# Kernel optimization log

Hardware: AMD Instinct MI355X
Metric: run time of the kernel (lower is better)

The kernel has to match this reference:

```python
import jax, jax.numpy as jnp
import numpy as np

B, L, D_MODEL, D_STATE, D_CONV, EXPAND = 2, 1024, 1024, 16, 4, 2
D_INNER = D_MODEL * EXPAND


def setup_inputs() -> dict:
    key = jax.random.key(0)
    ks = jax.random.split(key, 8)
    s = lambda fan: 1.0 / np.sqrt(fan)
    x = jax.random.normal(ks[0], (B, L, D_MODEL), jnp.float32)
    in_proj_w = jax.random.normal(ks[1], (D_MODEL, 2 * D_INNER), jnp.float32) * s(D_MODEL)
    conv_w = jax.random.normal(ks[2], (D_INNER, 1, D_CONV), jnp.float32) * s(D_CONV)
    conv_b = jax.random.normal(ks[3], (D_INNER,), jnp.float32) * 0.01
    x_proj_w = jax.random.normal(ks[4], (D_INNER, 2 * D_STATE + D_INNER), jnp.float32) * s(D_INNER)
    dt_proj_w = jax.random.normal(ks[5], (D_INNER, D_INNER), jnp.float32) * s(D_INNER)
    dt_proj_b = jax.random.normal(ks[6], (D_INNER,), jnp.float32) * 0.01
    A_log = jnp.log(jnp.tile(jnp.arange(1, D_STATE + 1, dtype=jnp.float32)[None, :], (D_INNER, 1)))
    D = jnp.ones((D_INNER,), jnp.float32)
    out_proj_w = jax.random.normal(ks[7], (D_INNER, D_MODEL), jnp.float32) * s(D_INNER)
    return {"x": x, "in_proj_w": in_proj_w, "conv_w": conv_w, "conv_b": conv_b,
            "x_proj_w": x_proj_w, "dt_proj_w": dt_proj_w, "dt_proj_b": dt_proj_b,
            "A_log": A_log, "D": D, "out_proj_w": out_proj_w}


def _mamba_forward(x, in_proj_w, conv_w, conv_b, x_proj_w, dt_proj_w, dt_proj_b, A_log, D, out_proj_w):
    Bb, Ll, _ = x.shape
    d_inner, _, d_conv = conv_w.shape
    d_state = A_log.shape[1]
    # input projection and gate split
    xz = x @ in_proj_w                       # [B, L, 2*Di]
    x_inner, z = jnp.split(xz, 2, axis=-1)   # each [B, L, Di]
    # causal depthwise conv (left pad k-1, truncate to L == torch pad+slice)
    xc = jnp.transpose(x_inner, (0, 2, 1))   # [B, Di, L]
    xc = jax.lax.conv_general_dilated(
        xc, conv_w, window_strides=(1,), padding=[(d_conv - 1, 0)],
        dimension_numbers=("NCH", "OIH", "NCH"), feature_group_count=d_inner)
    xc = xc + conv_b[None, :, None]
    u = jax.nn.silu(jnp.transpose(xc, (0, 2, 1)))  # [B, L, Di]
    # SSM parameter projections
    ssm = u @ x_proj_w                        # [B, L, 2N+Di]
    B_ssm = ssm[..., :d_state]                # [B, L, N]
    C_ssm = ssm[..., d_state:2 * d_state]     # [B, L, N]
    dt = jax.nn.softplus(ssm[..., 2 * d_state:] @ dt_proj_w + dt_proj_b)  # [B, L, Di]
    A_real = -jnp.exp(A_log)                  # [Di, N]
    # selective scan over sequence (recurrence via lax.scan)
    def step(h, inp):
        dt_t, B_t, u_t = inp                  # [B,Di], [B,N], [B,Di]
        dA = jnp.exp(dt_t[..., None] * A_real)            # [B, Di, N]
        dBu = dt_t[..., None] * B_t[:, None, :] * u_t[..., None]
        h = dA * h + dBu
        return h, h
    h0 = jnp.zeros((Bb, d_inner, d_state), x.dtype)
    xs = (jnp.swapaxes(dt, 0, 1), jnp.swapaxes(B_ssm, 0, 1), jnp.swapaxes(u, 0, 1))
    _, states = jax.lax.scan(step, h0, xs)    # [L, B, Di, N]
    y = jnp.einsum("lbdn,lbn->lbd", states, jnp.swapaxes(C_ssm, 0, 1))
    y = jnp.swapaxes(y, 0, 1) + D * u         # skip connection
    y = y * jax.nn.silu(z)                    # gating
    return y @ out_proj_w                     # [B, L, d_model]


def reference(x, in_proj_w, conv_w, conv_b, x_proj_w, dt_proj_w, dt_proj_b, A_log, D, out_proj_w):
    return _mamba_forward(x, in_proj_w, conv_w, conv_b, x_proj_w, dt_proj_w, dt_proj_b, A_log, D, out_proj_w)
```

## Files before the change

kernel.cpp:

```cpp
#include <hip/hip_runtime.h>
#include <hip/hip_bf16.h>

#define BB 2
#define LL 1024
#define DMODEL 1024
#define DINNER 2048
#define DSTATE 16
#define DCONV 4
#define MM (BB * LL)
#define N_XZ 4096
#define N_SSM 2080
#define N_SSM_PAD 2176
#define CCH 32
#define LCH 32

typedef __hip_bfloat16 bf16;
typedef short bf16x8 __attribute__((ext_vector_type(8)));
typedef float f32x4 __attribute__((ext_vector_type(4)));

__device__ __forceinline__ void load16_lds(const bf16* g, bf16* l) {
    __builtin_amdgcn_global_load_lds(
        (const __attribute__((address_space(1))) void*)g,
        (__attribute__((address_space(3))) void*)l,
        16, 0, 0);
}

__global__ void cvt_kernel(const float* __restrict__ in, bf16* __restrict__ out, int n) {
    int i = blockIdx.x * blockDim.x + threadIdx.x;
    if (i < n) out[i] = __float2bfloat16(in[i]);
}

__global__ void transpose_cvt_kernel(const float* __restrict__ in, bf16* __restrict__ out,
                                     int K, int N) {
    __shared__ float tile[32][33];
    const int nb = blockIdx.x * 32, kb = blockIdx.y * 32;
    const int tx = threadIdx.x & 31;
    const int ty = threadIdx.x >> 5;
    #pragma unroll
    for (int i = 0; i < 32; i += 8) {
        int k = kb + ty + i, n = nb + tx;
        tile[ty + i][tx] = (k < K && n < N) ? in[(size_t)k * N + n] : 0.f;
    }
    __syncthreads();
    #pragma unroll
    for (int i = 0; i < 32; i += 8) {
        int n = nb + ty + i, k = kb + tx;
        if (n < N && k < K) out[(size_t)n * K + k] = __float2bfloat16(tile[tx][ty + i]);
    }
}

#define TM 128
#define TN 64
#define TK 32
template<int EPI>
__global__ __launch_bounds__(256) void mfma_gemm(
    const bf16* __restrict__ A, int lda,
    const bf16* __restrict__ Wt, int ldw,
    float* __restrict__ Cf, bf16* __restrict__ Cb, int ldc,
    const float* __restrict__ bias,
    int N, int K)
{
    __shared__ __align__(16) bf16 As[TM * TK];
    __shared__ __align__(16) bf16 Bs[TN * TK];
    const int tid = threadIdx.x;
    const int wave = tid >> 6, lane = tid & 63;
    const int wm = (wave >> 1) * 64, wn = (wave & 1) * 32;
    const int m0 = blockIdx.y * TM, n0 = blockIdx.x * TN;
    const int lm = lane & 15;
    const int kq = lane >> 4;

    const int srow = lane >> 2;
    const int scol = (lane & 3) * 8;

    f32x4 acc[4][2] = {};

    const bf16* Aw0 = A + (size_t)(m0 + wave * 16 + srow) * lda + scol;
    const bf16* Aw1 = A + (size_t)(m0 + wave * 16 + 64 + srow) * lda + scol;
    const bf16* Bw  = Wt + (size_t)(n0 + wave * 16 + srow) * ldw + scol;
    bf16* As0 = &As[(wave * 16) * TK];
    bf16* As1 = &As[(wave * 16 + 64) * TK];
    bf16* Bs0 = &Bs[(wave * 16) * TK];

    for (int k0 = 0; k0 < K; k0 += TK) {
        load16_lds(Aw0 + k0, As0);
        load16_lds(Aw1 + k0, As1);
        load16_lds(Bw + k0, Bs0);
        __syncthreads();

        bf16x8 af[4], bfr[2];
        #pragma unroll
        for (int i = 0; i < 4; ++i)
            af[i] = *(const bf16x8*)(&As[(wm + i * 16 + lm) * TK + kq * 8]);
        #pragma unroll
        for (int j = 0; j < 2; ++j)
            bfr[j] = *(const bf16x8*)(&Bs[(wn + j * 16 + lm) * TK + kq * 8]);
        #pragma unroll
        for (int i = 0; i < 4; ++i)
            #pragma unroll
            for (int j = 0; j < 2; ++j)
                acc[i][j] = __builtin_amdgcn_mfma_f32_16x16x32_bf16(af[i], bfr[j], acc[i][j], 0, 0, 0);
        __syncthreads();
    }

    #pragma unroll
    for (int i = 0; i < 4; ++i) {
        #pragma unroll
        for (int j = 0; j < 2; ++j) {
            int gcol = n0 + wn + j * 16 + lm;
            if ((EPI == 0 || EPI == 3) && gcol >= N) continue;
            #pragma unroll
            for (int r = 0; r < 4; ++r) {
                int grow = m0 + wm + i * 16 + kq * 4 + r;
                float v = acc[i][j][r];
                if (EPI == 1) {
                    v += bias[gcol];
                    v = (v > 20.f) ? v : log1pf(__expf(v));
                    Cf[(size_t)grow * ldc + gcol] = v;
                } else if (EPI == 2) {
                    Cf[(size_t)grow * ldc + gcol] = v;
                } else if (EPI == 3) {
                    if (gcol < 32) Cf[(size_t)grow * 32 + gcol] = v;
                    else           Cb[(size_t)grow * ldc + gcol] = __float2bfloat16(v);
                } else {
                    Cb[(size_t)grow * ldc + gcol] = __float2bfloat16(v);
                }
            }
        }
    }
}

__global__ void conv_silu_kernel(const bf16* __restrict__ xz,
                                 const float* __restrict__ conv_w,
                                 const float* __restrict__ conv_b,
                                 bf16* __restrict__ u)
{
    int idx = blockIdx.x * blockDim.x + threadIdx.x;
    if (idx >= BB * LL * DINNER) return;
    int d = idx & (DINNER - 1);
    int l = (idx >> 11) & (LL - 1);
    int b = idx >> 21;
    float acc = conv_b[d];
    #pragma unroll
    for (int j = 0; j < DCONV; ++j) {
        int ll = l - (DCONV - 1) + j;
        if (ll >= 0) {
            float xv = (float)xz[((size_t)(b * LL + ll)) * N_XZ + d];
            acc = fmaf(conv_w[d * DCONV + j], xv, acc);
        }
    }
    u[idx] = __float2bfloat16(acc / (1.f + __expf(-acc)));
}

__global__ __launch_bounds__(256) void scan_phase_a(
    const float* __restrict__ dt, const bf16* __restrict__ u,
    const float* __restrict__ BC,
    const float* __restrict__ A_log,
    float* __restrict__ chunkP, float* __restrict__ chunkH)
{
    const int d = blockIdx.x * 256 + threadIdx.x;
    const int c = blockIdx.y, b = blockIdx.z;
    const int l0 = c * LCH;

    float A[DSTATE];
    {
        const f32x4* ap = (const f32x4*)(A_log + d * DSTATE);
        #pragma unroll
        for (int q = 0; q < 4; ++q) {
            f32x4 v = ap[q];
            #pragma unroll
            for (int r = 0; r < 4; ++r) A[q * 4 + r] = -__expf(v[r]);
        }
    }
    float h[DSTATE];
    #pragma unroll
    for (int n = 0; n < DSTATE; ++n) h[n] = 0.f;
    float sdt = 0.f;

    const float* dtp = dt + ((size_t)b * LL + l0) * DINNER + d;
    const bf16* up = u + ((size_t)b * LL + l0) * DINNER + d;
    const float* bcp = BC + ((size_t)b * LL + l0) * 32;

    #pragma unroll 2
    for (int i = 0; i < LCH; ++i) {
        float dtv = *dtp;
        float uv  = (float)*up;
        float du  = dtv * uv;
        f32x4 Bv[4];
        #pragma unroll
        for (int q = 0; q < 4; ++q) Bv[q] = *(const f32x4*)(bcp + q * 4);
        #pragma unroll
        for (int n = 0; n < DSTATE; ++n) {
            float a = __expf(dtv * A[n]);
            h[n] = fmaf(a, h[n], du * Bv[n >> 2][n & 3]);
        }
        sdt += dtv;
        dtp += DINNER; up += DINNER; bcp += 32;
    }

    size_t idx = (((size_t)b * CCH + c) * DINNER + d) * DSTATE;
    #pragma unroll
    for (int q = 0; q < 4; ++q) {
        f32x4 pv, hv;
        #pragma unroll
        for (int r = 0; r < 4; ++r) { pv[r] = __expf(A[q * 4 + r] * sdt); hv[r] = h[q * 4 + r]; }
        *(f32x4*)(chunkP + idx + q * 4) = pv;
        *(f32x4*)(chunkH + idx + q * 4) = hv;
    }
}

__global__ __launch_bounds__(256) void scan_phase_p(
    const float* __restrict__ chunkP, float* __restrict__ chunkH)
{
    int gid = blockIdx.x * 256 + threadIdx.x;
    int n = gid & 15;
    int d = (gid >> 4) & (DINNER - 1);
    int b = gid >> 15;
    const size_t stride = (size_t)DINNER * DSTATE;
    size_t idx = ((size_t)b * CCH * DINNER + d) * DSTATE + n;
    float H = 0.f;
    for (int c = 0; c < CCH; ++c) {
        float P  = chunkP[idx];
        float hl = chunkH[idx];
        chunkH[idx] = H;
        H = fmaf(P, H, hl);
        idx += stride;
    }
}

__global__ __launch_bounds__(256) void scan_phase_b(
    const float* __restrict__ dt, bf16* __restrict__ u,
    const float* __restrict__ BC, const bf16* __restrict__ xz,
    const float* __restrict__ A_log, const float* __restrict__ Dp,
    const float* __restrict__ chunkH)
{
    const int d = blockIdx.x * 256 + threadIdx.x;
    const int c = blockIdx.y, b = blockIdx.z;
    const int l0 = c * LCH;

    float A[DSTATE];
    {
        const f32x4* ap = (const f32x4*)(A_log + d * DSTATE);
        #pragma unroll
        for (int q = 0; q < 4; ++q) {
            f32x4 v = ap[q];
            #pragma unroll
            for (int r = 0; r < 4; ++r) A[q * 4 + r] = -__expf(v[r]);
        }
    }
    const float Dd = Dp[d];
    float h[DSTATE];
    {
        size_t idx = (((size_t)b * CCH + c) * DINNER + d) * DSTATE;
        #pragma unroll
        for (int q = 0; q < 4; ++q) {
            f32x4 v = *(const f32x4*)(chunkH + idx + q * 4);
            #pragma unroll
            for (int r = 0; r < 4; ++r) h[q * 4 + r] = v[r];
        }
    }

    const float* dtp = dt + ((size_t)b * LL + l0) * DINNER + d;
    bf16* up = u + ((size_t)b * LL + l0) * DINNER + d;
    const float* bcp = BC + ((size_t)b * LL + l0) * 32;
    const bf16* zp = xz + ((size_t)b * LL + l0) * N_XZ + DINNER + d;

    #pragma unroll 2
    for (int i = 0; i < LCH; ++i) {
        float dtv = *dtp;
        float uv  = (float)*up;
        float du  = dtv * uv;
        f32x4 Bv[4], Cv[4];
        #pragma unroll
        for (int q = 0; q < 4; ++q) {
            Bv[q] = *(const f32x4*)(bcp + q * 4);
            Cv[q] = *(const f32x4*)(bcp + 16 + q * 4);
        }
        float acc = 0.f;
        #pragma unroll
        for (int n = 0; n < DSTATE; ++n) {
            float a = __expf(dtv * A[n]);
            h[n] = fmaf(a, h[n], du * Bv[n >> 2][n & 3]);
            acc = fmaf(h[n], Cv[n >> 2][n & 3], acc);
        }
        float zv = (float)*zp;
        acc = fmaf(Dd, uv, acc);
        acc *= zv / (1.f + __expf(-zv));
        *up = __float2bfloat16(acc);
        dtp += DINNER; up += DINNER; bcp += 32; zp += N_XZ;
    }
}

extern "C" void kernel_launch(void* const* d_in, const int* in_sizes, int n_in,
                              void* d_out, int out_size, void* d_ws, size_t ws_size,
                              hipStream_t stream) {
    const float* x         = (const float*)d_in[0];
    const float* in_proj_w = (const float*)d_in[1];
    const float* conv_w    = (const float*)d_in[2];
    const float* conv_b    = (const float*)d_in[3];
    const float* x_proj_w  = (const float*)d_in[4];
    const float* dt_proj_w = (const float*)d_in[5];
    const float* dt_proj_b = (const float*)d_in[6];
    const float* A_log     = (const float*)d_in[7];
    const float* Dp        = (const float*)d_in[8];
    const float* out_proj_w= (const float*)d_in[9];
    float* out = (float*)d_out;

    char* p = (char*)d_ws;
    float* dt   = (float*)p;                          p += (size_t)MM * DINNER * 4;
    bf16*  xbf  = (bf16*)dt;
    bf16*  xz   = (bf16*)p;                           p += (size_t)MM * N_XZ * 2;
    bf16*  u    = (bf16*)p;                           p += (size_t)MM * DINNER * 2;
    bf16*  ssm  = (bf16*)p;                           p += (size_t)MM * N_SSM * 2;
    bf16*  Wt1  = (bf16*)p;                           p += (size_t)N_XZ * DMODEL * 2;
    bf16*  Wt2  = (bf16*)p;                           p += (size_t)N_SSM_PAD * DINNER * 2;
    bf16*  Wt3  = (bf16*)p;                           p += (size_t)DINNER * DINNER * 2;
    bf16*  Wt4  = (bf16*)p;                           p += (size_t)DMODEL * DINNER * 2;
    float* BC   = (float*)p;                          p += (size_t)MM * 32 * 4;
    float* chunkP = (float*)Wt1;
    float* chunkH = (float*)Wt2;

    {
        int n = MM * DMODEL;
        cvt_kernel<<<(n + 255) / 256, 256, 0, stream>>>(x, xbf, n);
        transpose_cvt_kernel<<<dim3(N_XZ / 32, DMODEL / 32), 256, 0, stream>>>(in_proj_w, Wt1, DMODEL, N_XZ);
        transpose_cvt_kernel<<<dim3((N_SSM + 31) / 32, DINNER / 32), 256, 0, stream>>>(x_proj_w, Wt2, DINNER, N_SSM);
        transpose_cvt_kernel<<<dim3(DINNER / 32, DINNER / 32), 256, 0, stream>>>(dt_proj_w, Wt3, DINNER, DINNER);
        transpose_cvt_kernel<<<dim3(DMODEL / 32, DINNER / 32), 256, 0, stream>>>(out_proj_w, Wt4, DINNER, DMODEL);
    }
    mfma_gemm<0><<<dim3(N_XZ / TN, MM / TM), 256, 0, stream>>>(
        xbf, DMODEL, Wt1, DMODEL, nullptr, xz, N_XZ, nullptr, N_XZ, DMODEL);
    {
        int n = BB * LL * DINNER;
        conv_silu_kernel<<<(n + 255) / 256, 256, 0, stream>>>(xz, conv_w, conv_b, u);
    }
    mfma_gemm<3><<<dim3(N_SSM_PAD / TN, MM / TM), 256, 0, stream>>>(
        u, DINNER, Wt2, DINNER, BC, ssm, N_SSM, nullptr, N_SSM, DINNER);
    mfma_gemm<1><<<dim3(DINNER / TN, MM / TM), 256, 0, stream>>>(
        ssm + 2 * DSTATE, N_SSM, Wt3, DINNER, dt, nullptr, DINNER, dt_proj_b, DINNER, DINNER);
    scan_phase_a<<<dim3(DINNER / 256, CCH, BB), 256, 0, stream>>>(dt, u, BC, A_log, chunkP, chunkH);
    scan_phase_p<<<dim3(BB * DINNER * DSTATE / 256), 256, 0, stream>>>(chunkP, chunkH);
    scan_phase_b<<<dim3(DINNER / 256, CCH, BB), 256, 0, stream>>>(dt, u, BC, xz, A_log, Dp, chunkH);
    mfma_gemm<2><<<dim3(DMODEL / TN, MM / TM), 256, 0, stream>>>(
        u, DINNER, Wt4, DINNER, out, nullptr, DMODEL, nullptr, DMODEL, DINNER);
}
```

Before: 378.1 us.

## Swizzle GEMM LDS layout and split-K the output projection with atomics

Adds an XOR-style rotation of the 8-element column groups used when staging A and B tiles into LDS, so that fragment reads hit fewer bank conflicts. The out-projection GEMM is also split along K into two halves using blockIdx.z. The output is zeroed with a memset and the partial sums are accumulated with float atomicAdd. This doubles the block count of the small 1024-wide GEMM to improve CU occupancy, at the cost of an extra memset, atomic traffic and nondeterministic summation order.

```diff
diff --git a/kernel.cpp b/kernel.cpp
--- a/kernel.cpp
+++ b/kernel.cpp
@@ -52,7 +52,7 @@
 #define TM 128
 #define TN 64
 #define TK 32
-template<int EPI>
+template<int EPI, int KSPLIT = 1>
 __global__ __launch_bounds__(256) void mfma_gemm(
     const bf16* __restrict__ A, int lda,
     const bf16* __restrict__ Wt, int ldw,
@@ -66,34 +66,38 @@
     const int wave = tid >> 6, lane = tid & 63;
     const int wm = (wave >> 1) * 64, wn = (wave & 1) * 32;
     const int m0 = blockIdx.y * TM, n0 = blockIdx.x * TN;
-    const int lm = lane & 15;
-    const int kq = lane >> 4;
+    const int lm = lane & 15, kq = lane >> 4;
 
     const int srow = lane >> 2;
-    const int scol = (lane & 3) * 8;
-
-    f32x4 acc[4][2] = {};
-
-    const bf16* Aw0 = A + (size_t)(m0 + wave * 16 + srow) * lda + scol;
-    const bf16* Aw1 = A + (size_t)(m0 + wave * 16 + 64 + srow) * lda + scol;
-    const bf16* Bw  = Wt + (size_t)(n0 + wave * 16 + srow) * ldw + scol;
+    const int cg = ((lane & 3) - ((srow >> 1) & 3)) & 3;
+    const bf16* gA0 = A + (size_t)(m0 + wave * 16 + srow) * lda + cg * 8;
+    const bf16* gA1 = A + (size_t)(m0 + wave * 16 + 64 + srow) * lda + cg * 8;
+    const bf16* gB  = Wt + (size_t)(n0 + wave * 16 + srow) * ldw + cg * 8;
     bf16* As0 = &As[(wave * 16) * TK];
     bf16* As1 = &As[(wave * 16 + 64) * TK];
     bf16* Bs0 = &Bs[(wave * 16) * TK];
 
-    for (int k0 = 0; k0 < K; k0 += TK) {
-        load16_lds(Aw0 + k0, As0);
-        load16_lds(Aw1 + k0, As1);
-        load16_lds(Bw + k0, Bs0);
+    const int soff = ((kq + ((lm >> 1) & 3)) & 3) * 8;
+
+    const int Kc = K / KSPLIT;
+    const int kbeg = (KSPLIT > 1) ? blockIdx.z * Kc : 0;
+
+    f32x4 acc[4][2] = {};
+
+    for (int it = 0; it < Kc; it += TK) {
+        const int k0 = kbeg + it;
+        load16_lds(gA0 + k0, As0);
+        load16_lds(gA1 + k0, As1);
+        load16_lds(gB + k0, Bs0);
         __syncthreads();
 
         bf16x8 af[4], bfr[2];
         #pragma unroll
         for (int i = 0; i < 4; ++i)
-            af[i] = *(const bf16x8*)(&As[(wm + i * 16 + lm) * TK + kq * 8]);
+            af[i] = *(const bf16x8*)(&As[(wm + i * 16 + lm) * TK + soff]);
         #pragma unroll
         for (int j = 0; j < 2; ++j)
-            bfr[j] = *(const bf16x8*)(&Bs[(wn + j * 16 + lm) * TK + kq * 8]);
+            bfr[j] = *(const bf16x8*)(&Bs[(wn + j * 16 + lm) * TK + soff]);
         #pragma unroll
         for (int i = 0; i < 4; ++i)
             #pragma unroll
@@ -117,7 +121,8 @@
                     v = (v > 20.f) ? v : log1pf(__expf(v));
                     Cf[(size_t)grow * ldc + gcol] = v;
                 } else if (EPI == 2) {
-                    Cf[(size_t)grow * ldc + gcol] = v;
+                    if (KSPLIT > 1) atomicAdd(&Cf[(size_t)grow * ldc + gcol], v);
+                    else            Cf[(size_t)grow * ldc + gcol] = v;
                 } else if (EPI == 3) {
                     if (gcol < 32) Cf[(size_t)grow * 32 + gcol] = v;
                     else           Cb[(size_t)grow * ldc + gcol] = __float2bfloat16(v);
@@ -340,6 +345,7 @@
     scan_phase_a<<<dim3(DINNER / 256, CCH, BB), 256, 0, stream>>>(dt, u, BC, A_log, chunkP, chunkH);
     scan_phase_p<<<dim3(BB * DINNER * DSTATE / 256), 256, 0, stream>>>(chunkP, chunkH);
     scan_phase_b<<<dim3(DINNER / 256, CCH, BB), 256, 0, stream>>>(dt, u, BC, xz, A_log, Dp, chunkH);
-    mfma_gemm<2><<<dim3(DMODEL / TN, MM / TM), 256, 0, stream>>>(
+    hipMemsetAsync(out, 0, (size_t)out_size * sizeof(float), stream);
+    mfma_gemm<2, 2><<<dim3(DMODEL / TN, MM / TM, 2), 256, 0, stream>>>(
         u, DINNER, Wt4, DINNER, out, nullptr, DMODEL, nullptr, DMODEL, DINNER);
 }
```

New measurement: 374.7 us. No clear change (-0.9%).
